# Kernel tuning notes

Measured on AMD Instinct MI355X. Metric: run time of the kernel, lower is better.

The kernel has to match this reference:

```python
import jax, jax.numpy as jnp
import numpy as np

N_ATOMS = 500_000
N_MOLS = 25_000
HID = 300
CONSTRAINT = 0.0  # per-molecule target total (e.g. neutral net charge)
W_SCALE = 0.05    # keep random-init activations tame


def setup_inputs() -> dict:
    key = jax.random.key(0)
    ks = jax.random.split(key, 6)
    hidden = jax.random.normal(ks[0], (N_ATOMS, HID), dtype=jnp.float32)
    seg_ids = jnp.sort(jax.random.randint(ks[1], (N_ATOMS,), 0, N_MOLS, dtype=jnp.int32))
    # output readout FFN: Linear(300->300) -> ReLU -> Linear(300->1)
    W1 = jax.random.normal(ks[2], (HID, HID), dtype=jnp.float32) * W_SCALE
    b1 = jnp.zeros((HID,), dtype=jnp.float32)
    W2 = jax.random.normal(ks[3], (HID, 1), dtype=jnp.float32) * W_SCALE
    b2 = jnp.zeros((1,), dtype=jnp.float32)
    # weights readout FFN (same architecture); bias=1 keeps segment weight sums positive
    V1 = jax.random.normal(ks[4], (HID, HID), dtype=jnp.float32) * W_SCALE
    vb1 = jnp.zeros((HID,), dtype=jnp.float32)
    V2 = jax.random.normal(ks[5], (HID, 1), dtype=jnp.float32) * W_SCALE
    vb2 = jnp.ones((1,), dtype=jnp.float32)
    return {"hidden": hidden, "seg_ids": seg_ids, "W1": W1, "b1": b1, "W2": W2,
            "b2": b2, "V1": V1, "vb1": vb1, "V2": V2, "vb2": vb2}


def _ffn(x, Wa, ba, Wb, bb):
    # dropout is identity in eval mode
    h = jax.nn.relu(x @ Wa + ba)
    return h @ Wb + bb  # [N, 1]


def reference(hidden, seg_ids, W1, b1, W2, b2, V1, vb1, V2, vb2):
    output = _ffn(hidden, W1, b1, W2, b2)    # [N, 1] raw per-atom predictions
    weights = _ffn(hidden, V1, vb1, V2, vb2) # [N, 1] per-atom correction weights
    # per-molecule segment sums (replaces the Python loop over a_scope)
    sum_o = jax.ops.segment_sum(output[:, 0], seg_ids, num_segments=N_MOLS)   # [M]
    sum_w = jax.ops.segment_sum(weights[:, 0], seg_ids, num_segments=N_MOLS)  # [M]
    sum_w = jnp.where(sum_w == 0, 1.0, sum_w)  # empty segments are skipped in the original
    corr = (CONSTRAINT - sum_o) / sum_w        # [M]
    out = output + weights * corr[seg_ids][:, None]  # [N, 1]
    return out
```

## Files before the change

kernel.cpp:

```cpp
#include <hip/hip_runtime.h>
#include <hip/hip_bf16.h>
#include <stdint.h>

#define N_ATOMS 500000
#define N_MOLS  25000
#define HID     300
#define BA      64
#define WS_ELE  102400
#define NCH     19
#define AROWB   616

typedef __attribute__((ext_vector_type(8)))  short          short8v;
typedef __attribute__((ext_vector_type(16))) float          f32x16;

static __device__ __forceinline__ unsigned short f2bf(float f) {
  unsigned int u = __float_as_uint(f);
  u += 0x7fffu + ((u >> 16) & 1u);
  return (unsigned short)(u >> 16);
}

__global__ void prep_kernel(
    const float* __restrict__ W1, const float* __restrict__ V1,
    const float* __restrict__ b1, const float* __restrict__ vb1,
    const float* __restrict__ W2, const float* __restrict__ V2,
    unsigned short* __restrict__ W1s, unsigned short* __restrict__ V1s,
    float* __restrict__ b1p, float* __restrict__ vb1p,
    float* __restrict__ W2p, float* __restrict__ V2p,
    float* __restrict__ sums)
{
  const int t = blockIdx.x * 256 + threadIdx.x;
  if (t < 2 * WS_ELE) {
    const float* src = (t < WS_ELE) ? W1 : V1;
    unsigned short* dst = (t < WS_ELE) ? W1s : V1s;
    const int i    = (t < WS_ELE) ? t : t - WS_ELE;
    const int j    = i & 7;
    const int lane = (i >> 3) & 63;
    const int nt   = (i >> 9) % 10;
    const int kc16 = i / 5120;
    const int k = kc16 * 16 + (lane >> 5) * 8 + j;
    const int n = nt * 32 + (lane & 31);
    const float v = (k < HID && n < HID) ? src[k * HID + n] : 0.f;
    dst[i] = f2bf(v);
  } else if (t < 2 * WS_ELE + 1280) {
    const int i = t - 2 * WS_ELE;
    const int which = i / 320;
    const int e = i - which * 320;
    const float* s = (which == 0) ? b1 : (which == 1) ? vb1 : (which == 2) ? W2 : V2;
    float*       d = (which == 0) ? b1p : (which == 1) ? vb1p : (which == 2) ? W2p : V2p;
    d[e] = (e < HID) ? s[e] : 0.f;
  } else if (t < 2 * WS_ELE + 1280 + 2 * N_MOLS) {
    sums[t - (2 * WS_ELE + 1280)] = 0.f;
  }
}

__global__ __launch_bounds__(256, 2) void fused_ffn(
    const float* __restrict__ hidden,
    const unsigned short* __restrict__ W1s, const unsigned short* __restrict__ V1s,
    const float* __restrict__ b1p, const float* __restrict__ vb1p,
    const float* __restrict__ W2p, const float* __restrict__ V2p,
    const float* __restrict__ b2, const float* __restrict__ vb2,
    float* __restrict__ outA, float* __restrict__ outW)
{
  __shared__ char ldsA[BA * AROWB];
  __shared__ float sOutA[BA];
  __shared__ float sOutW[BA];

  const int tid = (int)threadIdx.x;
  const int ln  = tid & 63;
  const int wv  = tid >> 6;
  const int mtx = wv & 1;
  const int ch  = wv >> 1;
  const int l31 = ln & 31;
  const int lh  = ln >> 5;
  const long base = (long)blockIdx.x * BA;

  #pragma unroll
  for (int bt = 0; bt < 2; ++bt) {
    const int nb = bt ? 9 : 10;
    float4 tmp[10];
    #pragma unroll
    for (int m = 0; m < 10; ++m) {
      if (m >= nb) break;
      const int i   = tid + (bt * 10 + m) * 256;
      const int row = i / 76;
      const int c4  = i - row * 76;
      float4 v = make_float4(0.f, 0.f, 0.f, 0.f);
      const long atom = base + row;
      if (c4 < 75 && atom < N_ATOMS)
        v = *reinterpret_cast<const float4*>(hidden + atom * (long)HID + c4 * 4);
      tmp[m] = v;
    }
    #pragma unroll
    for (int m = 0; m < 10; ++m) {
      if (m >= nb) break;
      const int i   = tid + (bt * 10 + m) * 256;
      const int row = i / 76;
      const int c4  = i - row * 76;
      ushort4 b;
      b.x = (unsigned short)__bfloat16_as_ushort(__float2bfloat16(tmp[m].x));
      b.y = (unsigned short)__bfloat16_as_ushort(__float2bfloat16(tmp[m].y));
      b.z = (unsigned short)__bfloat16_as_ushort(__float2bfloat16(tmp[m].z));
      b.w = (unsigned short)__bfloat16_as_ushort(__float2bfloat16(tmp[m].w));
      *reinterpret_cast<ushort4*>(ldsA + row * AROWB + c4 * 8) = b;
    }
  }
  __syncthreads();

  const char* bwave = (mtx ? (const char*)V1s : (const char*)W1s) + ch * 5120;
  const char* aB0 = ldsA + l31 * AROWB + lh * 16;
  const char* aB1 = aB0 + 32 * AROWB;

  f32x16 acc[2][5] = {};
  short8v bc[5], bn[5];
  #pragma unroll
  for (int nt = 0; nt < 5; ++nt)
    bc[nt] = *reinterpret_cast<const short8v*>(bwave + nt * 1024 + ln * 16);

  for (int c = 0; c < NCH; ++c) {
    if (c < NCH - 1) {
      const char* bsrc = bwave + (c + 1) * 10240;
      #pragma unroll
      for (int nt = 0; nt < 5; ++nt)
        bn[nt] = *reinterpret_cast<const short8v*>(bsrc + nt * 1024 + ln * 16);
    }
    const short8v a0 = *reinterpret_cast<const short8v*>(aB0 + c * 32);
    const short8v a1 = *reinterpret_cast<const short8v*>(aB1 + c * 32);
    #pragma unroll
    for (int nt = 0; nt < 5; ++nt) {
      acc[0][nt] = __builtin_amdgcn_mfma_f32_32x32x16_bf16(a0, bc[nt], acc[0][nt], 0, 0, 0);
      acc[1][nt] = __builtin_amdgcn_mfma_f32_32x32x16_bf16(a1, bc[nt], acc[1][nt], 0, 0, 0);
    }
    if (c < NCH - 1) {
      #pragma unroll
      for (int nt = 0; nt < 5; ++nt) bc[nt] = bn[nt];
    }
  }

  float bv[5], w2[5];
  const float* bbv = mtx ? vb1p : b1p;
  const float* ww2 = mtx ? V2p  : W2p;
  #pragma unroll
  for (int nt = 0; nt < 5; ++nt) {
    const int cix = ch * 160 + nt * 32 + l31;
    bv[nt] = bbv[cix];
    w2[nt] = ww2[cix];
  }
  if (tid < BA) { sOutA[tid] = 0.f; sOutW[tid] = 0.f; }
  __syncthreads();

  float* sOut = mtx ? sOutW : sOutA;
  #pragma unroll
  for (int rg = 0; rg < 2; ++rg) {
    #pragma unroll
    for (int r = 0; r < 16; ++r) {
      float s = 0.f;
      #pragma unroll
      for (int nt = 0; nt < 5; ++nt) {
        float x = fmaxf(acc[rg][nt][r] + bv[nt], 0.f);
        s = fmaf(x, w2[nt], s);
      }
      s += __shfl_xor(s, 1);
      s += __shfl_xor(s, 2);
      s += __shfl_xor(s, 4);
      s += __shfl_xor(s, 8);
      s += __shfl_xor(s, 16);
      if (l31 == 0) {
        const int row = rg * 32 + (r & 3) + 8 * (r >> 2) + 4 * lh;
        atomicAdd(&sOut[row], s);
      }
    }
  }
  __syncthreads();
  if (tid < BA) {
    const long atom = base + tid;
    if (atom < N_ATOMS) {
      outA[atom] = sOutA[tid] + b2[0];
      outW[atom] = sOutW[tid] + vb2[0];
    }
  }
}

__global__ void segsum_kernel(
    const float* __restrict__ outA, const float* __restrict__ outW,
    const int* __restrict__ seg,
    float* __restrict__ sum_o, float* __restrict__ sum_w)
{
  const long i0 = ((long)blockIdx.x * 256 + threadIdx.x) * 8;
  if (i0 >= N_ATOMS) return;
  const int4   s0 = *reinterpret_cast<const int4*>(seg + i0);
  const int4   s1 = *reinterpret_cast<const int4*>(seg + i0 + 4);
  const float4 o0 = *reinterpret_cast<const float4*>(outA + i0);
  const float4 o1 = *reinterpret_cast<const float4*>(outA + i0 + 4);
  const float4 w0 = *reinterpret_cast<const float4*>(outW + i0);
  const float4 w1 = *reinterpret_cast<const float4*>(outW + i0 + 4);
  const int   ss[8] = {s0.x, s0.y, s0.z, s0.w, s1.x, s1.y, s1.z, s1.w};
  const float oo[8] = {o0.x, o0.y, o0.z, o0.w, o1.x, o1.y, o1.z, o1.w};
  const float ww[8] = {w0.x, w0.y, w0.z, w0.w, w1.x, w1.y, w1.z, w1.w};
  int cur = ss[0];
  float ao = 0.f, aw = 0.f;
  #pragma unroll
  for (int j = 0; j < 8; ++j) {
    if (ss[j] != cur) {
      atomicAdd(&sum_o[cur], ao);
      atomicAdd(&sum_w[cur], aw);
      cur = ss[j]; ao = 0.f; aw = 0.f;
    }
    ao += oo[j]; aw += ww[j];
  }
  atomicAdd(&sum_o[cur], ao);
  atomicAdd(&sum_w[cur], aw);
}

__global__ void final_kernel(
    const float* __restrict__ outA, const float* __restrict__ outW,
    const int* __restrict__ seg,
    const float* __restrict__ sum_o, const float* __restrict__ sum_w,
    float* __restrict__ out)
{
  const long i0 = ((long)blockIdx.x * 256 + threadIdx.x) * 4;
  if (i0 >= N_ATOMS) return;
  const int4   s4 = *reinterpret_cast<const int4*>(seg + i0);
  const float4 o4 = *reinterpret_cast<const float4*>(outA + i0);
  const float4 w4 = *reinterpret_cast<const float4*>(outW + i0);
  const int   ss[4] = {s4.x, s4.y, s4.z, s4.w};
  const float oo[4] = {o4.x, o4.y, o4.z, o4.w};
  const float ww[4] = {w4.x, w4.y, w4.z, w4.w};
  float r[4];
  #pragma unroll
  for (int j = 0; j < 4; ++j) {
    const int s = ss[j];
    float sw = sum_w[s];
    sw = (sw == 0.f) ? 1.f : sw;
    const float corr = (0.f - sum_o[s]) / sw;
    r[j] = oo[j] + ww[j] * corr;
  }
  *reinterpret_cast<float4*>(out + i0) = make_float4(r[0], r[1], r[2], r[3]);
}

extern "C" void kernel_launch(void* const* d_in, const int* in_sizes, int n_in,
                              void* d_out, int out_size, void* d_ws, size_t ws_size,
                              hipStream_t stream)
{
  const float* hidden = (const float*)d_in[0];
  const int*   seg    = (const int*)d_in[1];
  const float* W1     = (const float*)d_in[2];
  const float* b1     = (const float*)d_in[3];
  const float* W2     = (const float*)d_in[4];
  const float* b2     = (const float*)d_in[5];
  const float* V1     = (const float*)d_in[6];
  const float* vb1    = (const float*)d_in[7];
  const float* V2     = (const float*)d_in[8];
  const float* vb2    = (const float*)d_in[9];

  char* ws = (char*)d_ws;
  float*          outA  = (float*)(ws + 0);
  float*          outW  = (float*)(ws + 2000000);
  float*          sum_o = (float*)(ws + 4000000);
  float*          sum_w = (float*)(ws + 4100000);
  unsigned short* W1s   = (unsigned short*)(ws + 4200000);
  unsigned short* V1s   = (unsigned short*)(ws + 4404800);
  float*          b1p   = (float*)(ws + 4609600);
  float*          vb1p  = (float*)(ws + 4610880);
  float*          W2p   = (float*)(ws + 4612160);
  float*          V2p   = (float*)(ws + 4613440);

  prep_kernel<<<1001, 256, 0, stream>>>(W1, V1, b1, vb1, W2, V2,
                                        W1s, V1s, b1p, vb1p, W2p, V2p, sum_o);

  const int nblk = (N_ATOMS + BA - 1) / BA;
  fused_ffn<<<nblk, 256, 0, stream>>>(hidden, W1s, V1s, b1p, vb1p, W2p, V2p,
                                      b2, vb2, outA, outW);

  segsum_kernel<<<(N_ATOMS / 8 + 255) / 256, 256, 0, stream>>>(outA, outW, seg,
                                                               sum_o, sum_w);

  final_kernel<<<(N_ATOMS / 4 + 255) / 256, 256, 0, stream>>>(outA, outW, seg,
                                                              sum_o, sum_w,
                                                              (float*)d_out);
}
```

Baseline: 513.1 us.

## Add producer-wave double-buffered global_load_lds pipeline for hidden tiles

Restructures the FFN kernel into 640-thread blocks where two producer waves stream raw fp32 hidden tiles into double-buffered LDS via global_load_lds. Eight consumer waves convert to bf16 on the fly and run MFMA, so each block processes 8 tiles of 64 atoms. Outputs are written with global atomics into buffers zeroed by the prep kernel. A padded tail copy handles the partial last tile. The aim is to overlap HBM loads with compute and drop the per-block load/convert stall, at the cost of fewer blocks, larger LDS use and global atomics.

Result: slower. 1.101 ms (+114.6%).

```diff
diff --git a/kernel.cpp b/kernel.cpp
--- a/kernel.cpp
+++ b/kernel.cpp
@@ -5,10 +5,11 @@
 #define N_ATOMS 500000
 #define N_MOLS  25000
 #define HID     300
-#define BA      64
 #define WS_ELE  102400
 #define NCH     19
-#define AROWB   616
+#define TILEB   76832
+#define NTPB    8
+#define NBLK    977
 
 typedef __attribute__((ext_vector_type(8)))  short          short8v;
 typedef __attribute__((ext_vector_type(16))) float          f32x16;
@@ -19,14 +20,31 @@
   return (unsigned short)(u >> 16);
 }
 
+static __device__ __forceinline__ short8v pack8(float4 a, float4 b) {
+  union { __hip_bfloat16 h[8]; short8v v; } u;
+  u.h[0] = __float2bfloat16(a.x); u.h[1] = __float2bfloat16(a.y);
+  u.h[2] = __float2bfloat16(a.z); u.h[3] = __float2bfloat16(a.w);
+  u.h[4] = __float2bfloat16(b.x); u.h[5] = __float2bfloat16(b.y);
+  u.h[6] = __float2bfloat16(b.z); u.h[7] = __float2bfloat16(b.w);
+  return u.v;
+}
+
+static __device__ __forceinline__ void stage16(const char* gsrc, char* ldst, int ln) {
+  __builtin_amdgcn_global_load_lds(
+      (const __attribute__((address_space(1))) void*)(gsrc + ln * 16),
+      (__attribute__((address_space(3))) void*)ldst, 16, 0, 0);
+}
+
 __global__ void prep_kernel(
+    const float* __restrict__ hidden,
     const float* __restrict__ W1, const float* __restrict__ V1,
     const float* __restrict__ b1, const float* __restrict__ vb1,
     const float* __restrict__ W2, const float* __restrict__ V2,
     unsigned short* __restrict__ W1s, unsigned short* __restrict__ V1s,
     float* __restrict__ b1p, float* __restrict__ vb1p,
     float* __restrict__ W2p, float* __restrict__ V2p,
-    float* __restrict__ sums)
+    float* __restrict__ sums, float* __restrict__ outAW,
+    float* __restrict__ tail)
 {
   const int t = blockIdx.x * 256 + threadIdx.x;
   if (t < 2 * WS_ELE) {
@@ -50,134 +68,146 @@
     d[e] = (e < HID) ? s[e] : 0.f;
   } else if (t < 2 * WS_ELE + 1280 + 2 * N_MOLS) {
     sums[t - (2 * WS_ELE + 1280)] = 0.f;
-  }
-}
-
-__global__ __launch_bounds__(256, 2) void fused_ffn(
-    const float* __restrict__ hidden,
+  } else if (t < 2 * WS_ELE + 1280 + 2 * N_MOLS + 2 * N_ATOMS) {
+    outAW[t - (2 * WS_ELE + 1280 + 2 * N_MOLS)] = 0.f;
+  } else if (t < 2 * WS_ELE + 1280 + 2 * N_MOLS + 2 * N_ATOMS + (TILEB / 4)) {
+    const int i = t - (2 * WS_ELE + 1280 + 2 * N_MOLS + 2 * N_ATOMS);
+    const long g = (long)(N_ATOMS - 32) * HID + i;
+    tail[i] = (g < (long)N_ATOMS * HID) ? hidden[g] : 0.f;
+  }
+}
+
+__global__ __launch_bounds__(640, 2) void fused_ffn(
+    const float* __restrict__ hidden, const float* __restrict__ tail,
     const unsigned short* __restrict__ W1s, const unsigned short* __restrict__ V1s,
     const float* __restrict__ b1p, const float* __restrict__ vb1p,
     const float* __restrict__ W2p, const float* __restrict__ V2p,
     const float* __restrict__ b2, const float* __restrict__ vb2,
     float* __restrict__ outA, float* __restrict__ outW)
 {
-  __shared__ char ldsA[BA * AROWB];
-  __shared__ float sOutA[BA];
-  __shared__ float sOutW[BA];
+  __shared__ char lds[2 * TILEB];
 
   const int tid = (int)threadIdx.x;
   const int ln  = tid & 63;
   const int wv  = tid >> 6;
+  const bool producer = (wv >= 8);
+  const long base = (long)blockIdx.x * (64 * NTPB);
+
+  int ntile = NTPB;
+  {
+    const long rem = (long)N_ATOMS - base;
+    if (rem < 64 * NTPB) ntile = (int)((rem + 63) >> 6);
+  }
+
+  const int p0 = (wv == 8) ? 0 : 38;
+  const int np = (wv == 8) ? 38 : 37;
+
   const int mtx = wv & 1;
-  const int ch  = wv >> 1;
+  const int ch  = (wv >> 1) & 1;
+  const int rg  = (wv >> 2) & 1;
   const int l31 = ln & 31;
   const int lh  = ln >> 5;
-  const long base = (long)blockIdx.x * BA;
-
-  #pragma unroll
-  for (int bt = 0; bt < 2; ++bt) {
-    const int nb = bt ? 9 : 10;
-    float4 tmp[10];
+  const char* bwave = (mtx ? (const char*)V1s : (const char*)W1s) + ch * 5120;
+
+  float bv[5], w2[5];
+  float biasadd = 0.f;
+  float* outP = mtx ? outW : outA;
+  if (!producer) {
+    const float* bbv = mtx ? vb1p : b1p;
+    const float* ww2 = mtx ? V2p  : W2p;
     #pragma unroll
-    for (int m = 0; m < 10; ++m) {
-      if (m >= nb) break;
-      const int i   = tid + (bt * 10 + m) * 256;
-      const int row = i / 76;
-      const int c4  = i - row * 76;
-      float4 v = make_float4(0.f, 0.f, 0.f, 0.f);
-      const long atom = base + row;
-      if (c4 < 75 && atom < N_ATOMS)
-        v = *reinterpret_cast<const float4*>(hidden + atom * (long)HID + c4 * 4);
-      tmp[m] = v;
+    for (int nt = 0; nt < 5; ++nt) {
+      const int cix = ch * 160 + nt * 32 + l31;
+      bv[nt] = bbv[cix];
+      w2[nt] = ww2[cix];
     }
+    if (ch == 0) biasadd = mtx ? vb2[0] : b2[0];
+  }
+
+#define TSRC(t) ((base + 64 * (t) + 64 <= (long)N_ATOMS)                       \
+                   ? (const char*)(hidden + (base + 64 * (t)) * HID)           \
+                   : (const char*)tail)
+
+  if (producer) {
+    const char* s = TSRC(0);
     #pragma unroll
-    for (int m = 0; m < 10; ++m) {
-      if (m >= nb) break;
-      const int i   = tid + (bt * 10 + m) * 256;
-      const int row = i / 76;
-      const int c4  = i - row * 76;
-      ushort4 b;
-      b.x = (unsigned short)__bfloat16_as_ushort(__float2bfloat16(tmp[m].x));
-      b.y = (unsigned short)__bfloat16_as_ushort(__float2bfloat16(tmp[m].y));
-      b.z = (unsigned short)__bfloat16_as_ushort(__float2bfloat16(tmp[m].z));
-      b.w = (unsigned short)__bfloat16_as_ushort(__float2bfloat16(tmp[m].w));
-      *reinterpret_cast<ushort4*>(ldsA + row * AROWB + c4 * 8) = b;
+    for (int r = 0; r < 38; ++r)
+      if (r < np) stage16(s + (p0 + r) * 1024, lds + (p0 + r) * 1024, ln);
+  }
+
+  for (int t = 0; t < ntile; ++t) {
+    char* cbuf = lds + (t & 1) * TILEB;
+    char* nbuf = lds + ((t + 1) & 1) * TILEB;
+
+    __builtin_amdgcn_s_barrier();
+    __builtin_amdgcn_sched_barrier(0);
+
+    if (producer) {
+      if (t + 1 < ntile) {
+        const char* s = TSRC(t + 1);
+        #pragma unroll
+        for (int r = 0; r < 38; ++r)
+          if (r < np) stage16(s + (p0 + r) * 1024, nbuf + (p0 + r) * 1024, ln);
+        if (wv == 8) asm volatile("s_waitcnt vmcnt(38)" ::: "memory");
+        else         asm volatile("s_waitcnt vmcnt(37)" ::: "memory");
+      } else {
+        asm volatile("s_waitcnt vmcnt(0)" ::: "memory");
+      }
     }
-  }
-  __syncthreads();
-
-  const char* bwave = (mtx ? (const char*)V1s : (const char*)W1s) + ch * 5120;
-  const char* aB0 = ldsA + l31 * AROWB + lh * 16;
-  const char* aB1 = aB0 + 32 * AROWB;
-
-  f32x16 acc[2][5] = {};
-  short8v bc[5], bn[5];
-  #pragma unroll
-  for (int nt = 0; nt < 5; ++nt)
-    bc[nt] = *reinterpret_cast<const short8v*>(bwave + nt * 1024 + ln * 16);
-
-  for (int c = 0; c < NCH; ++c) {
-    if (c < NCH - 1) {
-      const char* bsrc = bwave + (c + 1) * 10240;
+
+    __builtin_amdgcn_s_barrier();
+    __builtin_amdgcn_sched_barrier(0);
+
+    if (!producer) {
+      const char* aP = cbuf + (rg * 32 + l31) * 1200 + lh * 32;
+      f32x16 acc[5] = {};
+      short8v bc[5], bn[5];
       #pragma unroll
       for (int nt = 0; nt < 5; ++nt)
-        bn[nt] = *reinterpret_cast<const short8v*>(bsrc + nt * 1024 + ln * 16);
-    }
-    const short8v a0 = *reinterpret_cast<const short8v*>(aB0 + c * 32);
-    const short8v a1 = *reinterpret_cast<const short8v*>(aB1 + c * 32);
-    #pragma unroll
-    for (int nt = 0; nt < 5; ++nt) {
-      acc[0][nt] = __builtin_amdgcn_mfma_f32_32x32x16_bf16(a0, bc[nt], acc[0][nt], 0, 0, 0);
-      acc[1][nt] = __builtin_amdgcn_mfma_f32_32x32x16_bf16(a1, bc[nt], acc[1][nt], 0, 0, 0);
-    }
-    if (c < NCH - 1) {
+        bc[nt] = *reinterpret_cast<const short8v*>(bwave + nt * 1024 + ln * 16);
+
+      for (int c = 0; c < NCH; ++c) {
+        if (c < NCH - 1) {
+          const char* bsrc = bwave + (c + 1) * 10240;
+          #pragma unroll
+          for (int nt = 0; nt < 5; ++nt)
+            bn[nt] = *reinterpret_cast<const short8v*>(bsrc + nt * 1024 + ln * 16);
+        }
+        const float4 f0 = *reinterpret_cast<const float4*>(aP + c * 64);
+        const float4 f1 = *reinterpret_cast<const float4*>(aP + c * 64 + 16);
+        const short8v af = pack8(f0, f1);
+        #pragma unroll
+        for (int nt = 0; nt < 5; ++nt)
+          acc[nt] = __builtin_amdgcn_mfma_f32_32x32x16_bf16(af, bc[nt], acc[nt], 0, 0, 0);
+        if (c < NCH - 1) {
+          #pragma unroll
+          for (int nt = 0; nt < 5; ++nt) bc[nt] = bn[nt];
+        }
+      }
+
+      const long tb = base + 64 * t;
       #pragma unroll
-      for (int nt = 0; nt < 5; ++nt) bc[nt] = bn[nt];
-    }
-  }
-
-  float bv[5], w2[5];
-  const float* bbv = mtx ? vb1p : b1p;
-  const float* ww2 = mtx ? V2p  : W2p;
-  #pragma unroll
-  for (int nt = 0; nt < 5; ++nt) {
-    const int cix = ch * 160 + nt * 32 + l31;
-    bv[nt] = bbv[cix];
-    w2[nt] = ww2[cix];
-  }
-  if (tid < BA) { sOutA[tid] = 0.f; sOutW[tid] = 0.f; }
-  __syncthreads();
-
-  float* sOut = mtx ? sOutW : sOutA;
-  #pragma unroll
-  for (int rg = 0; rg < 2; ++rg) {
-    #pragma unroll
-    for (int r = 0; r < 16; ++r) {
-      float s = 0.f;
-      #pragma unroll
-      for (int nt = 0; nt < 5; ++nt) {
-        float x = fmaxf(acc[rg][nt][r] + bv[nt], 0.f);
-        s = fmaf(x, w2[nt], s);
-      }
-      s += __shfl_xor(s, 1);
-      s += __shfl_xor(s, 2);
-      s += __shfl_xor(s, 4);
-      s += __shfl_xor(s, 8);
-      s += __shfl_xor(s, 16);
-      if (l31 == 0) {
-        const int row = rg * 32 + (r & 3) + 8 * (r >> 2) + 4 * lh;
-        atomicAdd(&sOut[row], s);
+      for (int r = 0; r < 16; ++r) {
+        float s = 0.f;
+        #pragma unroll
+        for (int nt = 0; nt < 5; ++nt) {
+          float x = fmaxf(acc[nt][r] + bv[nt], 0.f);
+          s = fmaf(x, w2[nt], s);
+        }
+        s += __shfl_xor(s, 1);
+        s += __shfl_xor(s, 2);
+        s += __shfl_xor(s, 4);
+        s += __shfl_xor(s, 8);
+        s += __shfl_xor(s, 16);
+        if (l31 == 0) {
+          const int row = rg * 32 + (r & 3) + 8 * (r >> 2) + 4 * lh;
+          const long atom = tb + row;
+          if (atom < N_ATOMS) atomicAdd(&outP[atom], s + biasadd);
+        }
       }
     }
   }
-  __syncthreads();
-  if (tid < BA) {
-    const long atom = base + tid;
-    if (atom < N_ATOMS) {
-      outA[atom] = sOutA[tid] + b2[0];
-      outW[atom] = sOutW[tid] + vb2[0];
-    }
-  }
+#undef TSRC
 }
 
 __global__ void segsum_kernel(
@@ -263,13 +293,15 @@
   float*          vb1p  = (float*)(ws + 4610880);
   float*          W2p   = (float*)(ws + 4612160);
   float*          V2p   = (float*)(ws + 4613440);
-
-  prep_kernel<<<1001, 256, 0, stream>>>(W1, V1, b1, vb1, W2, V2,
-                                        W1s, V1s, b1p, vb1p, W2p, V2p, sum_o);
-
-  const int nblk = (N_ATOMS + BA - 1) / BA;
-  fused_ffn<<<nblk, 256, 0, stream>>>(hidden, W1s, V1s, b1p, vb1p, W2p, V2p,
-                                      b2, vb2, outA, outW);
+  float*          tailb = (float*)(ws + 4614720);
+
+  const int prep_threads = 2 * WS_ELE + 1280 + 2 * N_MOLS + 2 * N_ATOMS + (TILEB / 4);
+  prep_kernel<<<(prep_threads + 255) / 256, 256, 0, stream>>>(
+      hidden, W1, V1, b1, vb1, W2, V2,
+      W1s, V1s, b1p, vb1p, W2p, V2p, sum_o, outA, tailb);
+
+  fused_ffn<<<NBLK, 640, 0, stream>>>(hidden, tailb, W1s, V1s, b1p, vb1p,
+                                      W2p, V2p, b2, vb2, outA, outW);
 
   segsum_kernel<<<(N_ATOMS / 8 + 255) / 256, 256, 0, stream>>>(outA, outW, seg,
                                                                sum_o, sum_w);
```
